# Optimization experiments

Measured on AMD Instinct MI355X. Metric: run time of the kernel, lower is better.

Reference implementation:

```python
import jax, jax.numpy as jnp
import numpy as np

D_MODEL = 256   # c / input_dim
D_INNER = 512   # expand * d_model
D_STATE = 16
DT_RANK = 16    # ceil(d_model / 16)
D_CONV = 3


def setup_inputs() -> dict:
    key = jax.random.key(0)
    ks = jax.random.split(key, 8)
    s = lambda k, shape, sc=0.02: (jax.random.normal(k, shape, jnp.float32) * sc)
    feature = jax.random.normal(ks[0], (16, D_MODEL, 32, 32), jnp.float32)
    A_init = jnp.broadcast_to(jnp.arange(1, D_STATE + 1, dtype=jnp.float32), (D_INNER, D_STATE))
    return {
        "feature": feature,
        "norm_w": jnp.ones((D_MODEL,), jnp.float32),                 # RMSNorm weight
        "w_in": s(ks[1], (D_MODEL, 2 * D_INNER)),                     # in_proj (no bias)
        "conv_w": s(ks[2], (D_INNER, D_CONV), 0.1),                   # depthwise conv kernel
        "conv_b": jnp.zeros((D_INNER,), jnp.float32),                 # conv bias
        "w_xproj": s(ks[3], (D_INNER, DT_RANK + 2 * D_STATE)),        # x_proj (no bias)
        "w_dt": s(ks[4], (DT_RANK, D_INNER)),                         # dt_proj weight
        "b_dt": s(ks[5], (D_INNER,), 0.1),                            # dt_proj bias
        "A_log": jnp.log(A_init),                                     # [d_inner, d_state]
        "D": jnp.ones((D_INNER,), jnp.float32),                       # skip param
        "w_out": s(ks[6], (D_INNER, D_MODEL)),                        # out_proj (no bias)
    }


def _mamba_residual(x, norm_w, w_in, conv_w, conv_b, w_xproj, w_dt, b_dt, A_log, D, w_out):
    # x: [B, L, d_model] where B = h*w (spatial positions) and L = original batch b
    B, L, _ = x.shape
    # RMSNorm
    xn = x * jax.lax.rsqrt(jnp.mean(x * x, axis=-1, keepdims=True) + 1e-5) * norm_w
    # input projection -> [B, L, 2*d_inner]
    xr = xn @ w_in
    xm, res = jnp.split(xr, 2, axis=-1)
    # depthwise causal conv1d along L
    xc = jnp.transpose(xm, (0, 2, 1))                 # [B, d_inner, L]
    k = conv_w[:, None, :]                             # [d_inner, 1, d_conv]
    xc = jax.lax.conv_general_dilated(
        xc, k, window_strides=(1,), padding=[(D_CONV - 1, 0)],
        feature_group_count=D_INNER)
    xc = xc + conv_b[None, :, None]
    xm = jax.nn.silu(jnp.transpose(xc, (0, 2, 1)))    # [B, L, d_inner]
    # selective SSM
    A = -jnp.exp(A_log)                                # [d_inner, d_state]
    dbc = xm @ w_xproj                                 # [B, L, dt_rank + 2*d_state]
    delta, Bm, Cm = jnp.split(dbc, [DT_RANK, DT_RANK + D_STATE], axis=-1)
    delta = jax.nn.softplus(delta @ w_dt + b_dt)       # [B, L, d_inner]
    dA = jnp.exp(delta[..., None] * A)                 # [B, L, d_inner, d_state]
    dBu = delta[..., None] * Bm[:, :, None, :] * xm[..., None]

    def step(h, inp):
        dA_t, dBu_t, C_t = inp                         # [B,d,n], [B,d,n], [B,n]
        h = dA_t * h + dBu_t
        y = jnp.einsum('bdn,bn->bd', h, C_t)
        return h, y

    h0 = jnp.zeros((B, D_INNER, D_STATE), xm.dtype)
    _, ys = jax.lax.scan(
        step, h0,
        (dA.transpose(1, 0, 2, 3), dBu.transpose(1, 0, 2, 3), Cm.transpose(1, 0, 2)))
    y = ys.transpose(1, 0, 2) + xm * D                 # [B, L, d_inner]
    y = y * jax.nn.silu(res)
    return y @ w_out + x                               # residual add


def reference(feature, norm_w, w_in, conv_w, conv_b, w_xproj, w_dt, b_dt, A_log, D, w_out):
    b, c, h, w = feature.shape
    # [b,c,h,w] -> [h*w, b, c]: Mamba batch = spatial positions, seq = samples
    x = feature.transpose(0, 2, 3, 1).reshape(b, h * w, c).transpose(1, 0, 2)
    out = _mamba_residual(x, norm_w, w_in, conv_w, conv_b, w_xproj, w_dt, b_dt, A_log, D, w_out)
    out = out.transpose(1, 0, 2).reshape(b, h, w, c).transpose(0, 3, 1, 2)
    return out
```

## Files before the change

### kernel.cpp

```cpp
#include <hip/hip_runtime.h>
#include <hip/hip_bf16.h>
#include <math.h>

#define NPOS   1024
#define NSAMP  16
#define DMODEL 256
#define DINNER 512
#define DSTATE 16
#define DTRANK 16
#define MROWS  (NPOS*NSAMP)
#define LOG2E  1.44269504f

typedef __attribute__((ext_vector_type(8))) short short8;
typedef __attribute__((ext_vector_type(4))) float f32x4;

__device__ __forceinline__ unsigned short f2bf(float f) {
    unsigned int u = __builtin_bit_cast(unsigned int, f);
    u = u + 0x7FFFu + ((u >> 16) & 1u);
    return (unsigned short)(u >> 16);
}
__device__ __forceinline__ float bf2f(short b) {
    unsigned int u = ((unsigned int)(unsigned short)b) << 16;
    return __builtin_bit_cast(float, u);
}
__device__ __forceinline__ void unpk(unsigned int v, float& a, float& b) {
    a = __builtin_bit_cast(float, v << 16);
    b = __builtin_bit_cast(float, v & 0xffff0000u);
}
__device__ __forceinline__ float fsilu(float x) {
    return x * __builtin_amdgcn_rcpf(1.f + __expf(-x));
}
__device__ __forceinline__ void gl16(const void* g, void* l) {
    __builtin_amdgcn_global_load_lds((const __attribute__((address_space(1))) void*)g,
                                     (__attribute__((address_space(3))) void*)l, 16, 0, 0);
}

__global__ __launch_bounds__(256) void kprep2(const float* __restrict__ feat,
                                              const float* __restrict__ norm_w,
                                              const float* __restrict__ w_in,
                                              const float* __restrict__ w_out,
                                              const float* __restrict__ w_xproj,
                                              const float* __restrict__ A_log,
                                              unsigned short* __restrict__ xnT,
                                              unsigned short* __restrict__ w_inT,
                                              unsigned short* __restrict__ w_outT,
                                              unsigned short* __restrict__ wxT,
                                              float2* __restrict__ scanc) {
    __shared__ float part[4][64];
    __shared__ float ssc[64];
    __shared__ char shmem[64 * 520];
    int b = blockIdx.x, t = threadIdx.x;
    if (b < 256) {
        int s = b & 15, p0 = (b >> 4) * 64;
        int pl = t & 63, cg = t >> 6;
        const float* base = feat + (size_t)s * (DMODEL * NPOS) + p0 + pl;
        float vals[64];
        float ss = 0.f;
        #pragma unroll
        for (int j = 0; j < 64; ++j) {
            float v = base[(size_t)(cg * 64 + j) * NPOS];
            vals[j] = v;
            ss += v * v;
        }
        part[cg][pl] = ss;
        __syncthreads();
        if (t < 64) {
            float tot = part[0][t] + part[1][t] + part[2][t] + part[3][t];
            ssc[t] = rsqrtf(tot * (1.f / DMODEL) + 1e-5f);
        }
        __syncthreads();
        float sc = ssc[pl];
        unsigned short* trow = (unsigned short*)(shmem + pl * 520);
        #pragma unroll
        for (int j = 0; j < 64; ++j)
            trow[cg * 64 + j] = f2bf(vals[j] * sc * norm_w[cg * 64 + j]);
        __syncthreads();
        int p = t >> 2, cb = (t & 3) * 64;
        const unsigned short* srow = (const unsigned short*)(shmem + p * 520);
        unsigned short* orow = xnT + (size_t)((s << 10) + p0 + p) * DMODEL + cb;
        #pragma unroll
        for (int j8 = 0; j8 < 8; ++j8) {
            short8 v;
            #pragma unroll
            for (int jj = 0; jj < 8; ++jj) v[jj] = srow[cb + j8 * 8 + jj];
            *reinterpret_cast<short8*>(orow + j8 * 8) = v;
        }
    } else if (b < 352) {
        const float* src; unsigned short* dst; int K, N, tk, tn;
        if (b < 320) { int tb = b - 256; src = w_in;  dst = w_inT;  K = 256; N = 1024; tk = tb >> 4; tn = tb & 15; }
        else         { int tb = b - 320; src = w_out; dst = w_outT; K = 512; N = 256;  tk = tb >> 2; tn = tb & 3;  }
        unsigned short (*tile)[65] = (unsigned short (*)[65])shmem;
        #pragma unroll
        for (int j = 0; j < 16; ++j) {
            int kl = j * 4 + (t >> 6), nl = t & 63;
            tile[kl][nl] = f2bf(src[(size_t)(tk * 64 + kl) * N + tn * 64 + nl]);
        }
        __syncthreads();
        #pragma unroll
        for (int j = 0; j < 16; ++j) {
            int nl = j * 4 + (t >> 6), kl = t & 63;
            dst[(size_t)(tn * 64 + nl) * K + tk * 64 + kl] = tile[kl][nl];
        }
    } else if (b < 448) {
        int idx = (b - 352) * 256 + t;
        int j = idx >> 9, k = idx & 511;
        wxT[idx] = f2bf(w_xproj[(size_t)k * 48 + j]);
    } else {
        #pragma unroll
        for (int dd = 0; dd < 2; ++dd) {
            int d = t + dd * 256;
            float Ar0 = -__expf(A_log[d * DSTATE]);
            bool geo = true;
            #pragma unroll
            for (int n = 1; n < DSTATE; ++n) {
                float An = -__expf(A_log[d * DSTATE + n]);
                geo = geo && (fabsf(An - (n + 1) * Ar0) <= 1e-4f * (n + 1));
            }
            scanc[d] = make_float2(LOG2E * Ar0, geo ? 1.f : 0.f);
        }
    }
}

__global__ __launch_bounds__(256) void k1_mfma(const unsigned short* __restrict__ xnT,
                                               const unsigned short* __restrict__ w_inT,
                                               unsigned short* __restrict__ xmbf,
                                               unsigned short* __restrict__ gbf) {
    __shared__ char As[128 * 128];
    __shared__ char Bs[128 * 128];
    int t = threadIdx.x;
    int m0 = blockIdx.y * 128, n0 = blockIdx.x * 128;
    int l = t & 63, w = t >> 6;
    int wm = w & 1, wn = w >> 1, g = l >> 4, lr = l & 15;

    f32x4 acc[4][4] = {};
    for (int k0 = 0; k0 < DMODEL; k0 += 64) {
        if (k0) __syncthreads();
        #pragma unroll
        for (int q = 0; q < 4; ++q) {
            int chunk = q * 256 + t;
            int row = chunk >> 3, cb = chunk & 7;
            gl16(xnT  + (size_t)(m0 + row) * DMODEL + k0 + cb * 8, As + chunk * 16);
            gl16(w_inT + (size_t)(n0 + row) * DMODEL + k0 + cb * 8, Bs + chunk * 16);
        }
        __syncthreads();
        #pragma unroll
        for (int ks = 0; ks < 2; ++ks) {
            short8 a[4], b[4];
            #pragma unroll
            for (int mi = 0; mi < 4; ++mi)
                a[mi] = *reinterpret_cast<short8*>(As + (wm * 64 + mi * 16 + lr) * 128 + ks * 64 + g * 16);
            #pragma unroll
            for (int ni = 0; ni < 4; ++ni)
                b[ni] = *reinterpret_cast<short8*>(Bs + (wn * 64 + ni * 16 + lr) * 128 + ks * 64 + g * 16);
            #pragma unroll
            for (int mi = 0; mi < 4; ++mi)
                #pragma unroll
                for (int ni = 0; ni < 4; ++ni)
                    acc[mi][ni] = __builtin_amdgcn_mfma_f32_16x16x32_bf16(a[mi], b[ni], acc[mi][ni], 0, 0, 0);
        }
    }
    bool isRes = (n0 >= 512);
    #pragma unroll
    for (int mi = 0; mi < 4; ++mi) {
        #pragma unroll
        for (int r = 0; r < 4; ++r) {
            int m = m0 + wm * 64 + mi * 16 + g * 4 + r;
            #pragma unroll
            for (int ni = 0; ni < 4; ++ni) {
                int n = n0 + wn * 64 + ni * 16 + lr;
                float v = acc[mi][ni][r];
                if (isRes) gbf[(size_t)m * DINNER + n - 512] = f2bf(fsilu(v));
                else       xmbf[(size_t)m * DINNER + n] = f2bf(v);
            }
        }
    }
}

__global__ __launch_bounds__(256) void uker(const unsigned short* __restrict__ xmbf,
                                            const float* __restrict__ conv_w,
                                            const float* __restrict__ conv_b,
                                            unsigned short* __restrict__ ubf) {
    int f = blockIdx.x * 256 + threadIdx.x;
    int m = f >> 6, dd0 = (f & 63) << 3;
    int s = m >> 10;
    const unsigned short* r0 = xmbf + (size_t)m * DINNER + dd0;
    short8 x0 = *reinterpret_cast<const short8*>(r0);
    short8 x1 = {}, x2 = {};
    if (s >= 1) x1 = *reinterpret_cast<const short8*>(r0 - 1024 * DINNER);
    if (s >= 2) x2 = *reinterpret_cast<const short8*>(r0 - 2048 * DINNER);
    float wv[24], cb8[8];
    #pragma unroll
    for (int q = 0; q < 6; ++q)
        *reinterpret_cast<float4*>(&wv[q * 4]) = *reinterpret_cast<const float4*>(conv_w + dd0 * 3 + q * 4);
    *reinterpret_cast<float4*>(&cb8[0]) = *reinterpret_cast<const float4*>(conv_b + dd0);
    *reinterpret_cast<float4*>(&cb8[4]) = *reinterpret_cast<const float4*>(conv_b + dd0 + 4);
    short8 v;
    #pragma unroll
    for (int j = 0; j < 8; ++j) {
        float cv = cb8[j] + wv[3 * j + 2] * bf2f(x0[j]) + wv[3 * j + 1] * bf2f(x1[j]) + wv[3 * j] * bf2f(x2[j]);
        v[j] = (short)f2bf(fsilu(cv));
    }
    *reinterpret_cast<short8*>(ubf + (size_t)m * DINNER + dd0) = v;
}

__global__ __launch_bounds__(256) void k3_mfma(const unsigned short* __restrict__ ubf,
                                               const unsigned short* __restrict__ wxT,
                                               float* __restrict__ dbc) {
    __shared__ char Ws[48 * 128];
    __shared__ char Xs[64 * 128];
    int t = threadIdx.x;
    int m0 = blockIdx.x * 64;
    int l = t & 63, w = t >> 6, g = l >> 4, lr = l & 15;
    f32x4 acc[3] = {};
    for (int k0 = 0; k0 < DINNER; k0 += 64) {
        if (k0) __syncthreads();
        #pragma unroll
        for (int q = 0; q < 4; ++q) {
            int c = q * 256 + t;
            if (c < 384) {
                int row = c >> 3, cb = c & 7;
                gl16(wxT + (size_t)row * DINNER + k0 + cb * 8, Ws + c * 16);
            } else if (c < 896) {
                int c2 = c - 384;
                int row = c2 >> 3, cb = c2 & 7;
                gl16(ubf + (size_t)(m0 + row) * DINNER + k0 + cb * 8, Xs + c2 * 16);
            }
        }
        __syncthreads();
        #pragma unroll
        for (int ks = 0; ks < 2; ++ks) {
            short8 bfr = *reinterpret_cast<short8*>(Xs + (w * 16 + lr) * 128 + ks * 64 + g * 16);
            #pragma unroll
            for (int aj = 0; aj < 3; ++aj) {
                short8 a = *reinterpret_cast<short8*>(Ws + (aj * 16 + lr) * 128 + ks * 64 + g * 16);
                acc[aj] = __builtin_amdgcn_mfma_f32_16x16x32_bf16(a, bfr, acc[aj], 0, 0, 0);
            }
        }
    }
    int mc = m0 + w * 16 + lr;
    #pragma unroll
    for (int aj = 0; aj < 3; ++aj)
        *reinterpret_cast<f32x4*>(dbc + (size_t)mc * 48 + aj * 16 + g * 4) = acc[aj];
}

__global__ __launch_bounds__(256) void k5_scan(const unsigned int* __restrict__ ubf2,
                                               const unsigned int* __restrict__ gbf2,
                                               const float* __restrict__ dbc,
                                               const float2* __restrict__ scanc,
                                               const float* __restrict__ w_dt,
                                               const float* __restrict__ b_dt,
                                               const float* __restrict__ A_log,
                                               const float* __restrict__ Dp,
                                               unsigned int* __restrict__ ybf2) {
    int p = blockIdx.x, t = threadIdx.x;
    int d0 = 2 * t, d1 = d0 + 1;
    float2 s0c = scanc[d0], s1c = scanc[d1];
    float c00 = s0c.x, c01 = s1c.x;
    bool geo = (s0c.y > 0.5f) && (s1c.y > 0.5f);
    float2 Dv = *reinterpret_cast<const float2*>(Dp + d0);
    float2 bdt = *reinterpret_cast<const float2*>(b_dt + d0);
    float wdt0[16], wdt1[16];
    #pragma unroll
    for (int r = 0; r < 16; ++r) {
        float2 wv = *reinterpret_cast<const float2*>(w_dt + r * DINNER + d0);
        wdt0[r] = wv.x; wdt1[r] = wv.y;
    }
    float h0[16], h1[16];
    #pragma unroll
    for (int n = 0; n < 16; ++n) { h0[n] = 0.f; h1[n] = 0.f; }
    unsigned int base = p * 256 + t;
    float bcA[32], bcB[32];
    unsigned int uA, gA, uB, gB;
    float dA0, dA1, dB0, dB1;

#define LOADBC(BUF, DL0, DL1, S) { \
    const float* rp = dbc + (size_t)((((S) << 10) + p) * 48); \
    float t0[16]; \
    _Pragma("unroll") for (int j = 0; j < 4; ++j) *reinterpret_cast<float4*>(&t0[j * 4]) = *reinterpret_cast<const float4*>(rp + j * 4); \
    _Pragma("unroll") for (int j = 0; j < 8; ++j) *reinterpret_cast<float4*>(&BUF[j * 4]) = *reinterpret_cast<const float4*>(rp + 16 + j * 4); \
    float dp0 = bdt.x, dp1 = bdt.y; \
    _Pragma("unroll") for (int r = 0; r < 16; ++r) { dp0 += t0[r] * wdt0[r]; dp1 += t0[r] * wdt1[r]; } \
    DL0 = (dp0 > 20.f) ? dp0 : __logf(1.f + __expf(dp0)); \
    DL1 = (dp1 > 20.f) ? dp1 : __logf(1.f + __expf(dp1)); }
#define LOADPF(U, G, S) { unsigned int o = ((unsigned int)(S) << 18) + base; U = ubf2[o]; G = gbf2[o]; }
#define STEP(S, BC, U, G, DL0, DL1) { \
    float u0, u1, g0, g1; unpk(U, u0, u1); unpk(G, g0, g1); \
    float du0 = DL0 * u0, du1 = DL1 * u1; float yv0 = 0.f, yv1 = 0.f; \
    if (geo) { \
        float r0 = exp2f(DL0 * c00), r1 = exp2f(DL1 * c01); \
        float rr0 = r0, rr1 = r1; \
        _Pragma("unroll") for (int n = 0; n < 16; ++n) { \
            h0[n] = rr0 * h0[n] + du0 * BC[n]; yv0 += h0[n] * BC[16 + n]; rr0 *= r0; \
            h1[n] = rr1 * h1[n] + du1 * BC[n]; yv1 += h1[n] * BC[16 + n]; rr1 *= r1; } \
    } else { \
        _Pragma("unroll") for (int n = 0; n < 16; ++n) { \
            float An0 = -__expf(A_log[d0 * 16 + n]); float An1 = -__expf(A_log[d1 * 16 + n]); \
            h0[n] = __expf(DL0 * An0) * h0[n] + du0 * BC[n]; yv0 += h0[n] * BC[16 + n]; \
            h1[n] = __expf(DL1 * An1) * h1[n] + du1 * BC[n]; yv1 += h1[n] * BC[16 + n]; } \
    } \
    unsigned int o = ((unsigned int)(S) << 18) + base; \
    ybf2[o] = ((unsigned int)f2bf((yv1 + u1 * Dv.y) * g1) << 16) | f2bf((yv0 + u0 * Dv.x) * g0); }

    LOADBC(bcA, dA0, dA1, 0); LOADPF(uA, gA, 0);
    #pragma unroll
    for (int it = 0; it < 8; ++it) {
        int sa = 2 * it, sb = 2 * it + 1;
        int sn = (2 * it + 2 < 16) ? 2 * it + 2 : 15;
        LOADBC(bcB, dB0, dB1, sb); LOADPF(uB, gB, sb);
        STEP(sa, bcA, uA, gA, dA0, dA1);
        LOADBC(bcA, dA0, dA1, sn); LOADPF(uA, gA, sn);
        STEP(sb, bcB, uB, gB, dB0, dB1);
    }
#undef LOADBC
#undef LOADPF
#undef STEP
}

__global__ __launch_bounds__(256) void k6_mfma(const unsigned short* __restrict__ ybf,
                                               const unsigned short* __restrict__ w_outT,
                                               const float* __restrict__ feat,
                                               float* __restrict__ out) {
    __shared__ char As[128 * 128];
    __shared__ char Bs[128 * 128];
    int t = threadIdx.x;
    int m0 = blockIdx.x * 128;
    int cblk = blockIdx.y * 128;
    int s = m0 >> 10, p0 = m0 & 1023;
    int l = t & 63, w = t >> 6;
    int wm = w & 1, wn = w >> 1, g = l >> 4, lr = l & 15;

    f32x4 acc[4][4] = {};
    for (int k0 = 0; k0 < DINNER; k0 += 64) {
        if (k0) __syncthreads();
        #pragma unroll
        for (int q = 0; q < 4; ++q) {
            int chunk = q * 256 + t;
            int row = chunk >> 3, cb = chunk & 7;
            gl16(w_outT + (size_t)(cblk + row) * DINNER + k0 + cb * 8, As + chunk * 16);
            gl16(ybf    + (size_t)(m0 + row) * DINNER + k0 + cb * 8, Bs + chunk * 16);
        }
        __syncthreads();
        #pragma unroll
        for (int ks = 0; ks < 2; ++ks) {
            short8 a[4], b[4];
            #pragma unroll
            for (int mi = 0; mi < 4; ++mi)
                a[mi] = *reinterpret_cast<short8*>(As + (wm * 64 + mi * 16 + lr) * 128 + ks * 64 + g * 16);
            #pragma unroll
            for (int ni = 0; ni < 4; ++ni)
                b[ni] = *reinterpret_cast<short8*>(Bs + (wn * 64 + ni * 16 + lr) * 128 + ks * 64 + g * 16);
            #pragma unroll
            for (int mi = 0; mi < 4; ++mi)
                #pragma unroll
                for (int ni = 0; ni < 4; ++ni)
                    acc[mi][ni] = __builtin_amdgcn_mfma_f32_16x16x32_bf16(a[mi], b[ni], acc[mi][ni], 0, 0, 0);
        }
    }
    #pragma unroll
    for (int mi = 0; mi < 4; ++mi) {
        #pragma unroll
        for (int r = 0; r < 4; ++r) {
            int c = cblk + wm * 64 + mi * 16 + g * 4 + r;
            #pragma unroll
            for (int ni = 0; ni < 4; ++ni) {
                int p = p0 + wn * 64 + ni * 16 + lr;
                size_t idx = (size_t)s * (DMODEL * NPOS) + (size_t)c * NPOS + p;
                out[idx] = acc[mi][ni][r] + feat[idx];
            }
        }
    }
}

extern "C" void kernel_launch(void* const* d_in, const int* in_sizes, int n_in,
                              void* d_out, int out_size, void* d_ws, size_t ws_size,
                              hipStream_t stream) {
    const float* feature = (const float*)d_in[0];
    const float* norm_w  = (const float*)d_in[1];
    const float* w_in    = (const float*)d_in[2];
    const float* conv_w  = (const float*)d_in[3];
    const float* conv_b  = (const float*)d_in[4];
    const float* w_xproj = (const float*)d_in[5];
    const float* w_dt    = (const float*)d_in[6];
    const float* b_dt    = (const float*)d_in[7];
    const float* A_log   = (const float*)d_in[8];
    const float* Dp      = (const float*)d_in[9];
    const float* w_out   = (const float*)d_in[10];
    float* out = (float*)d_out;

    char* ws = (char*)d_ws;
    unsigned short* xnT    = (unsigned short*)(ws + 0);
    unsigned short* xmbf   = (unsigned short*)(ws + 8388608);
    unsigned short* gbf    = (unsigned short*)(ws + 25165824);
    float*          dbc    = (float*)(ws + 41943040);
    unsigned short* ubf    = (unsigned short*)(ws + 45088768);
    unsigned short* ybf    = (unsigned short*)(ws + 61865984);
    unsigned short* w_inT  = (unsigned short*)(ws + 78643200);
    unsigned short* w_outT = (unsigned short*)(ws + 79167488);
    unsigned short* wxT    = (unsigned short*)(ws + 79429632);
    float2*         scanc  = (float2*)(ws + 79478784);

    kprep2<<<449, 256, 0, stream>>>(feature, norm_w, w_in, w_out, w_xproj, A_log,
                                    xnT, w_inT, w_outT, wxT, scanc);
    k1_mfma<<<dim3(1024 / 128, MROWS / 128), 256, 0, stream>>>(xnT, w_inT, xmbf, gbf);
    uker<<<(MROWS * DINNER / 8) / 256, 256, 0, stream>>>(xmbf, conv_w, conv_b, ubf);
    k3_mfma<<<MROWS / 64, 256, 0, stream>>>(ubf, wxT, dbc);
    k5_scan<<<NPOS, 256, 0, stream>>>((const unsigned int*)ubf, (const unsigned int*)gbf,
                                      dbc, scanc, w_dt, b_dt, A_log, Dp, (unsigned int*)ybf);
    k6_mfma<<<dim3(MROWS / 128, DMODEL / 128), 256, 0, stream>>>(ybf, w_outT, feature, out);
}
```

Measured before the change: 187.6 us.

## Fuse causal conv+SiLU into x_proj GEMM and enlarge in_proj M tile

Removes the separate conv kernel by computing the depthwise causal conv and SiLU while staging the x_proj GEMM operand tile. The result goes to LDS for the MFMA and to global memory for the scan. This saves one launch and one read of the activation before x_proj. Separately, the in_proj GEMM now uses 512-thread blocks with 256-row M tiles, so each B tile is reused by more rows. The trade-offs are synchronous global loads in the GEMM producer path and more LDS and threads per block in k1.

```diff
diff --git a/kernel.cpp b/kernel.cpp
--- a/kernel.cpp
+++ b/kernel.cpp
@@ -121,26 +121,29 @@
     }
 }
 
-__global__ __launch_bounds__(256) void k1_mfma(const unsigned short* __restrict__ xnT,
+__global__ __launch_bounds__(512) void k1_mfma(const unsigned short* __restrict__ xnT,
                                                const unsigned short* __restrict__ w_inT,
                                                unsigned short* __restrict__ xmbf,
                                                unsigned short* __restrict__ gbf) {
-    __shared__ char As[128 * 128];
+    __shared__ char As[256 * 128];
     __shared__ char Bs[128 * 128];
     int t = threadIdx.x;
-    int m0 = blockIdx.y * 128, n0 = blockIdx.x * 128;
+    int m0 = blockIdx.y * 256, n0 = blockIdx.x * 128;
     int l = t & 63, w = t >> 6;
-    int wm = w & 1, wn = w >> 1, g = l >> 4, lr = l & 15;
+    int wm = w & 3, wn = w >> 2, g = l >> 4, lr = l & 15;
 
     f32x4 acc[4][4] = {};
     for (int k0 = 0; k0 < DMODEL; k0 += 64) {
         if (k0) __syncthreads();
         #pragma unroll
         for (int q = 0; q < 4; ++q) {
-            int chunk = q * 256 + t;
-            int row = chunk >> 3, cb = chunk & 7;
-            gl16(xnT  + (size_t)(m0 + row) * DMODEL + k0 + cb * 8, As + chunk * 16);
-            gl16(w_inT + (size_t)(n0 + row) * DMODEL + k0 + cb * 8, Bs + chunk * 16);
+            int c = q * 512 + t;
+            gl16(xnT + (size_t)(m0 + (c >> 3)) * DMODEL + k0 + (c & 7) * 8, As + c * 16);
+        }
+        #pragma unroll
+        for (int q = 0; q < 2; ++q) {
+            int c = q * 512 + t;
+            gl16(w_inT + (size_t)(n0 + (c >> 3)) * DMODEL + k0 + (c & 7) * 8, Bs + c * 16);
         }
         __syncthreads();
         #pragma unroll
@@ -176,55 +179,47 @@
     }
 }
 
-__global__ __launch_bounds__(256) void uker(const unsigned short* __restrict__ xmbf,
-                                            const float* __restrict__ conv_w,
-                                            const float* __restrict__ conv_b,
-                                            unsigned short* __restrict__ ubf) {
-    int f = blockIdx.x * 256 + threadIdx.x;
-    int m = f >> 6, dd0 = (f & 63) << 3;
-    int s = m >> 10;
-    const unsigned short* r0 = xmbf + (size_t)m * DINNER + dd0;
-    short8 x0 = *reinterpret_cast<const short8*>(r0);
-    short8 x1 = {}, x2 = {};
-    if (s >= 1) x1 = *reinterpret_cast<const short8*>(r0 - 1024 * DINNER);
-    if (s >= 2) x2 = *reinterpret_cast<const short8*>(r0 - 2048 * DINNER);
-    float wv[24], cb8[8];
-    #pragma unroll
-    for (int q = 0; q < 6; ++q)
-        *reinterpret_cast<float4*>(&wv[q * 4]) = *reinterpret_cast<const float4*>(conv_w + dd0 * 3 + q * 4);
-    *reinterpret_cast<float4*>(&cb8[0]) = *reinterpret_cast<const float4*>(conv_b + dd0);
-    *reinterpret_cast<float4*>(&cb8[4]) = *reinterpret_cast<const float4*>(conv_b + dd0 + 4);
-    short8 v;
-    #pragma unroll
-    for (int j = 0; j < 8; ++j) {
-        float cv = cb8[j] + wv[3 * j + 2] * bf2f(x0[j]) + wv[3 * j + 1] * bf2f(x1[j]) + wv[3 * j] * bf2f(x2[j]);
-        v[j] = (short)f2bf(fsilu(cv));
-    }
-    *reinterpret_cast<short8*>(ubf + (size_t)m * DINNER + dd0) = v;
-}
-
-__global__ __launch_bounds__(256) void k3_mfma(const unsigned short* __restrict__ ubf,
+__global__ __launch_bounds__(256) void k3_mfma(const unsigned short* __restrict__ xmbf,
+                                               const float* __restrict__ conv_w,
+                                               const float* __restrict__ conv_b,
                                                const unsigned short* __restrict__ wxT,
-                                               float* __restrict__ dbc) {
+                                               float* __restrict__ dbc,
+                                               unsigned short* __restrict__ ubf) {
     __shared__ char Ws[48 * 128];
     __shared__ char Xs[64 * 128];
     int t = threadIdx.x;
     int m0 = blockIdx.x * 64;
+    int s = m0 >> 10;
     int l = t & 63, w = t >> 6, g = l >> 4, lr = l & 15;
     f32x4 acc[3] = {};
     for (int k0 = 0; k0 < DINNER; k0 += 64) {
         if (k0) __syncthreads();
-        #pragma unroll
-        for (int q = 0; q < 4; ++q) {
+        for (int c = t; c < 384; c += 256)
+            gl16(wxT + (size_t)(c >> 3) * DINNER + k0 + (c & 7) * 8, Ws + c * 16);
+        #pragma unroll
+        for (int q = 0; q < 2; ++q) {
             int c = q * 256 + t;
-            if (c < 384) {
-                int row = c >> 3, cb = c & 7;
-                gl16(wxT + (size_t)row * DINNER + k0 + cb * 8, Ws + c * 16);
-            } else if (c < 896) {
-                int c2 = c - 384;
-                int row = c2 >> 3, cb = c2 & 7;
-                gl16(ubf + (size_t)(m0 + row) * DINNER + k0 + cb * 8, Xs + c2 * 16);
+            int row = c >> 3, cb = c & 7;
+            int m = m0 + row, d0 = k0 + cb * 8;
+            const unsigned short* r0 = xmbf + (size_t)m * DINNER + d0;
+            short8 x0 = *reinterpret_cast<const short8*>(r0);
+            short8 x1 = {}, x2 = {};
+            if (s >= 1) x1 = *reinterpret_cast<const short8*>(r0 - 1024 * DINNER);
+            if (s >= 2) x2 = *reinterpret_cast<const short8*>(r0 - 2048 * DINNER);
+            float wv[24], cb8[8];
+            #pragma unroll
+            for (int qq = 0; qq < 6; ++qq)
+                *reinterpret_cast<float4*>(&wv[qq * 4]) = *reinterpret_cast<const float4*>(conv_w + d0 * 3 + qq * 4);
+            *reinterpret_cast<float4*>(&cb8[0]) = *reinterpret_cast<const float4*>(conv_b + d0);
+            *reinterpret_cast<float4*>(&cb8[4]) = *reinterpret_cast<const float4*>(conv_b + d0 + 4);
+            short8 v;
+            #pragma unroll
+            for (int j = 0; j < 8; ++j) {
+                float cv = cb8[j] + wv[3 * j + 2] * bf2f(x0[j]) + wv[3 * j + 1] * bf2f(x1[j]) + wv[3 * j] * bf2f(x2[j]);
+                v[j] = (short)f2bf(fsilu(cv));
             }
+            *reinterpret_cast<short8*>(Xs + c * 16) = v;
+            *reinterpret_cast<short8*>(ubf + (size_t)m * DINNER + d0) = v;
         }
         __syncthreads();
         #pragma unroll
@@ -401,9 +396,8 @@
 
     kprep2<<<449, 256, 0, stream>>>(feature, norm_w, w_in, w_out, w_xproj, A_log,
                                     xnT, w_inT, w_outT, wxT, scanc);
-    k1_mfma<<<dim3(1024 / 128, MROWS / 128), 256, 0, stream>>>(xnT, w_inT, xmbf, gbf);
-    uker<<<(MROWS * DINNER / 8) / 256, 256, 0, stream>>>(xmbf, conv_w, conv_b, ubf);
-    k3_mfma<<<MROWS / 64, 256, 0, stream>>>(ubf, wxT, dbc);
+    k1_mfma<<<dim3(1024 / 128, MROWS / 256), 512, 0, stream>>>(xnT, w_inT, xmbf, gbf);
+    k3_mfma<<<MROWS / 64, 256, 0, stream>>>(xmbf, conv_w, conv_b, wxT, dbc, ubf);
     k5_scan<<<NPOS, 256, 0, stream>>>((const unsigned int*)ubf, (const unsigned int*)gbf,
                                       dbc, scanc, w_dt, b_dt, A_log, Dp, (unsigned int*)ybf);
     k6_mfma<<<dim3(MROWS / 128, DMODEL / 128), 256, 0, stream>>>(ybf, w_outT, feature, out);
```

Measured after the change: 200.0 us. 6.6% more time.
